# Kernel optimization log

Measured on AMD Instinct MI355X. Metric: run time of the kernel, lower is better.

The kernel has to match this reference:

```python
import jax, jax.numpy as jnp
import numpy as np

N_QUBITS = 4
DIM = 2 ** N_QUBITS  # 16
B = 262144
N_FEATURES = 64


def _apply_ry(state, theta, q):
    # state: (B, 16) complex64; theta: scalar or (B,) angle; RY on wire q (wire 0 = MSB)
    b = state.shape[0]
    L, R = 2 ** q, 2 ** (N_QUBITS - 1 - q)
    s = state.reshape(b, L, 2, R)
    theta = jnp.broadcast_to(jnp.asarray(theta, jnp.float32), (b,))
    c = jnp.cos(theta * 0.5)[:, None, None]
    sn = jnp.sin(theta * 0.5)[:, None, None]
    s0, s1 = s[:, :, 0], s[:, :, 1]
    n0 = c * s0 - sn * s1
    n1 = sn * s0 + c * s1
    return jnp.stack([n0, n1], axis=2).reshape(b, DIM)


def _apply_rz(state, theta, q):
    # RZ(theta) = diag(exp(-i theta/2), exp(+i theta/2)) on wire q
    b = state.shape[0]
    L, R = 2 ** q, 2 ** (N_QUBITS - 1 - q)
    s = state.reshape(b, L, 2, R)
    theta = jnp.broadcast_to(jnp.asarray(theta, jnp.float32), (b,))
    p = jnp.exp(-0.5j * theta)[:, None, None].astype(state.dtype)
    n0 = s[:, :, 0] * p
    n1 = s[:, :, 1] * jnp.conj(p)
    return jnp.stack([n0, n1], axis=2).reshape(b, DIM)


def _cnot(state, c):
    # CNOT with control wire c, target wire c+1 (adjacent, as in the circuit)
    b = state.shape[0]
    L, R = 2 ** c, 2 ** (N_QUBITS - 2 - c)
    s = state.reshape(b, L, 2, 2, R)
    s1 = jnp.flip(s[:, :, 1], axis=2)  # flip target when control=1
    return jnp.stack([s[:, :, 0], s1], axis=2).reshape(b, DIM)


def _simulate(angles, w):
    # angles: (B, 4) input RY rotations; w: (8, 2) trainable gate angles
    b = angles.shape[0]
    state = jnp.zeros((b, DIM), jnp.complex64).at[:, 0].set(1.0)
    for q in range(N_QUBITS):
        state = _apply_ry(state, angles[:, q], q)
    for q in range(N_QUBITS):
        state = _apply_rz(state, w[q, 0], q)
        state = _apply_ry(state, w[q, 1], q)
    for q in range(N_QUBITS - 1):
        state = _cnot(state, q)
    for q in range(N_QUBITS):
        state = _apply_rz(state, w[q + N_QUBITS, 0], q)
        state = _apply_ry(state, w[q + N_QUBITS, 1], q)
    probs = (state.real ** 2 + state.imag ** 2).reshape((b,) + (2,) * N_QUBITS)
    outs = []
    for q in range(N_QUBITS):
        axes = tuple(a for a in range(1, N_QUBITS + 1) if a != q + 1)
        p = probs.sum(axis=axes)  # (B, 2)
        outs.append(p[:, 0] - p[:, 1])  # <Z_q>
    return jnp.stack(outs, axis=1).astype(jnp.float32)


def setup_inputs() -> dict:
    key = jax.random.key(0)
    k1, k2, k3 = jax.random.split(key, 3)
    x = jax.random.normal(k1, (B, N_FEATURES), jnp.float32)
    fm_w = jax.random.normal(k2, (N_QUBITS, N_FEATURES), jnp.float32) / jnp.sqrt(N_FEATURES)
    fm_b = jnp.zeros((N_QUBITS,), jnp.float32)
    # TorchLayer default init: uniform(0, 2*pi)
    q_weights = jax.random.uniform(k3, (2 * N_QUBITS, 2), jnp.float32, 0.0, 2.0 * np.pi)
    return {"x": x, "fm_w": fm_w, "fm_b": fm_b, "q_weights": q_weights}


def reference(x, fm_w, fm_b, q_weights):
    angles = x @ fm_w.T + fm_b  # feature_map Linear(n_features -> n_qubits)
    return _simulate(angles, q_weights)  # (B, n_qubits) Pauli-Z expectations
```

## Files before the change

kernel.cpp:

```cpp
#include <hip/hip_runtime.h>

#define NQ 4
#define DIM 16
#define NPAIR 136

__global__ __launch_bounds__(256) void qnn_prep(const float* __restrict__ w,
                                                float* __restrict__ Apack) {
    __shared__ float Ure[DIM][DIM + 1];
    __shared__ float Uim[DIM][DIM + 1];
    const int tid = threadIdx.x;

    if (tid < DIM) {
        float re[DIM], im[DIM];
#pragma unroll
        for (int k = 0; k < DIM; ++k) { re[k] = (k == tid) ? 1.f : 0.f; im[k] = 0.f; }

#pragma unroll
        for (int layer = 0; layer < 2; ++layer) {
#pragma unroll
            for (int q = 0; q < NQ; ++q) {
                const int bit = 1 << (3 - q);
                const int g = layer * NQ + q;
                float sr, cr;
                sincosf(0.5f * w[g * 2 + 0], &sr, &cr);
#pragma unroll
                for (int k = 0; k < DIM; ++k) {
                    if (!(k & bit)) {
                        const int k1 = k | bit;
                        float r0 = re[k], i0 = im[k], r1 = re[k1], i1 = im[k1];
                        re[k]  = r0 * cr + i0 * sr;  im[k]  = i0 * cr - r0 * sr;
                        re[k1] = r1 * cr - i1 * sr;  im[k1] = i1 * cr + r1 * sr;
                    }
                }
                float sy, cy;
                sincosf(0.5f * w[g * 2 + 1], &sy, &cy);
#pragma unroll
                for (int k = 0; k < DIM; ++k) {
                    if (!(k & bit)) {
                        const int k1 = k | bit;
                        float r0 = re[k], i0 = im[k], r1 = re[k1], i1 = im[k1];
                        re[k]  = cy * r0 - sy * r1;  im[k]  = cy * i0 - sy * i1;
                        re[k1] = sy * r0 + cy * r1;  im[k1] = sy * i0 + cy * i1;
                    }
                }
            }
            if (layer == 0) {
#pragma unroll
                for (int c = 0; c < 3; ++c) {
                    const int cb = 1 << (3 - c), tb = 1 << (2 - c);
#pragma unroll
                    for (int k = 0; k < DIM; ++k) {
                        if ((k & cb) && !(k & tb)) {
                            const int k1 = k | tb;
                            float t;
                            t = re[k]; re[k] = re[k1]; re[k1] = t;
                            t = im[k]; im[k] = im[k1]; im[k1] = t;
                        }
                    }
                }
            }
        }
#pragma unroll
        for (int k = 0; k < DIM; ++k) { Ure[k][tid] = re[k]; Uim[k][tid] = im[k]; }
    }
    __syncthreads();

    if (tid < NPAIR) {
        int i = 0, j = 0, pp = tid;
        for (i = 0; i < DIM; ++i) {
            const int row = DIM - i;
            if (pp < row) { j = i + pp; break; }
            pp -= row;
        }
        const float f = (i == j) ? 1.f : 2.f;
#pragma unroll
        for (int q = 0; q < NQ; ++q) {
            float acc = 0.f;
#pragma unroll
            for (int k = 0; k < DIM; ++k) {
                const float zq = ((k >> (3 - q)) & 1) ? -1.f : 1.f;
                acc += zq * (Ure[k][i] * Ure[k][j] + Uim[k][i] * Uim[k][j]);
            }
            Apack[tid * 4 + q] = f * acc;
        }
    }
}

__global__ __launch_bounds__(256) void qnn_main(const float* __restrict__ x,
                                                const float* __restrict__ fm_w,
                                                const float* __restrict__ fm_b,
                                                const float* __restrict__ Apack,
                                                float* __restrict__ out, int B) {
    const int b = blockIdx.x * 256 + threadIdx.x;
    if (b >= B) return;

    float acc[NQ];
#pragma unroll
    for (int q = 0; q < NQ; ++q) acc[q] = fm_b[q];

    const float4* __restrict__ x4 = (const float4*)(x + (size_t)b * 64);
    const float4* __restrict__ w4 = (const float4*)fm_w;
#pragma unroll
    for (int t = 0; t < 16; ++t) {
        const float4 xv = x4[t];
#pragma unroll
        for (int q = 0; q < NQ; ++q) {
            const float4 wv = w4[q * 16 + t];
            acc[q] += xv.x * wv.x + xv.y * wv.y + xv.z * wv.z + xv.w * wv.w;
        }
    }

    float c[NQ], s[NQ];
#pragma unroll
    for (int q = 0; q < NQ; ++q) __sincosf(0.5f * acc[q], &s[q], &c[q]);

    float p01[4], p23[4];
#pragma unroll
    for (int u = 0; u < 4; ++u) {
        p01[u] = ((u & 2) ? s[0] : c[0]) * ((u & 1) ? s[1] : c[1]);
        p23[u] = ((u & 2) ? s[2] : c[2]) * ((u & 1) ? s[3] : c[3]);
    }
    float st[DIM];
#pragma unroll
    for (int i = 0; i < DIM; ++i) st[i] = p01[i >> 2] * p23[i & 3];

    float o0 = 0.f, o1 = 0.f, o2 = 0.f, o3 = 0.f;
    const float4* __restrict__ A4 = (const float4*)Apack;
    int p = 0;
#pragma unroll
    for (int i = 0; i < DIM; ++i) {
#pragma unroll
        for (int j = i; j < DIM; ++j) {
            const float pr = st[i] * st[j];
            const float4 aq = A4[p];
            o0 += aq.x * pr; o1 += aq.y * pr; o2 += aq.z * pr; o3 += aq.w * pr;
            ++p;
        }
    }

    float4 o = make_float4(o0, o1, o2, o3);
    *(float4*)(out + (size_t)b * 4) = o;
}

extern "C" void kernel_launch(void* const* d_in, const int* in_sizes, int n_in,
                              void* d_out, int out_size, void* d_ws, size_t ws_size,
                              hipStream_t stream) {
    const float* x    = (const float*)d_in[0];
    const float* fm_w = (const float*)d_in[1];
    const float* fm_b = (const float*)d_in[2];
    const float* qw   = (const float*)d_in[3];
    float* out = (float*)d_out;
    float* Apack = (float*)d_ws;

    const int B = in_sizes[0] / 64;

    qnn_prep<<<1, 256, 0, stream>>>(qw, Apack);
    qnn_main<<<(B + 255) / 256, 256, 0, stream>>>(x, fm_w, fm_b, Apack, out, B);
}
```

Measured before the change: 29.16 us.

## Stage x tile through LDS with coalesced float4 loads per block

Each 128-thread block now loads its 128x64 slice of x with coalesced float4 reads across threads, stores it into padded shared memory, then each thread reads its own row from LDS. Before this, each thread loaded a 256-byte contiguous row, so lanes in a wavefront touched addresses far apart. The block size also drops from 256 to 128. The cost is about 34 KB of LDS per block, which may limit occupancy, plus a barrier and extra registers to hold the staged float4s.

```diff
diff --git a/kernel.cpp b/kernel.cpp
--- a/kernel.cpp
+++ b/kernel.cpp
@@ -3,6 +3,8 @@
 #define NQ 4
 #define DIM 16
 #define NPAIR 136
+#define ROWS 128
+#define XPAD 68
 
 __global__ __launch_bounds__(256) void qnn_prep(const float* __restrict__ w,
                                                 float* __restrict__ Apack) {
@@ -86,23 +88,48 @@
     }
 }
 
-__global__ __launch_bounds__(256) void qnn_main(const float* __restrict__ x,
+__global__ __launch_bounds__(128) void qnn_main(const float* __restrict__ x,
                                                 const float* __restrict__ fm_w,
                                                 const float* __restrict__ fm_b,
                                                 const float* __restrict__ Apack,
                                                 float* __restrict__ out, int B) {
-    const int b = blockIdx.x * 256 + threadIdx.x;
+    __shared__ float xs[ROWS * XPAD];
+    const int tid = threadIdx.x;
+    const long long tile = (long long)blockIdx.x * ROWS;
+
+    const float4* __restrict__ xg = (const float4*)(x + tile * 64);
+    const long long rem = (long long)B - tile;
+    float4 r[16];
+    if (rem >= ROWS) {
+#pragma unroll
+        for (int i = 0; i < 16; ++i) r[i] = xg[tid + 128 * i];
+    } else {
+#pragma unroll
+        for (int i = 0; i < 16; ++i) {
+            const int v = tid + 128 * i;
+            r[i] = (v < (int)rem * 16) ? xg[v] : make_float4(0.f, 0.f, 0.f, 0.f);
+        }
+    }
+#pragma unroll
+    for (int i = 0; i < 16; ++i) {
+        const int v = tid + 128 * i;
+        const int rw = v >> 4, c4 = v & 15;
+        *(float4*)&xs[rw * XPAD + c4 * 4] = r[i];
+    }
+    __syncthreads();
+
+    const long long b = tile + tid;
     if (b >= B) return;
 
     float acc[NQ];
 #pragma unroll
     for (int q = 0; q < NQ; ++q) acc[q] = fm_b[q];
 
-    const float4* __restrict__ x4 = (const float4*)(x + (size_t)b * 64);
+    const float4* __restrict__ xr = (const float4*)&xs[tid * XPAD];
     const float4* __restrict__ w4 = (const float4*)fm_w;
 #pragma unroll
     for (int t = 0; t < 16; ++t) {
-        const float4 xv = x4[t];
+        const float4 xv = xr[t];
 #pragma unroll
         for (int q = 0; q < NQ; ++q) {
             const float4 wv = w4[q * 16 + t];
@@ -138,8 +165,7 @@
         }
     }
 
-    float4 o = make_float4(o0, o1, o2, o3);
-    *(float4*)(out + (size_t)b * 4) = o;
+    *(float4*)(out + b * 4) = make_float4(o0, o1, o2, o3);
 }
 
 extern "C" void kernel_launch(void* const* d_in, const int* in_sizes, int n_in,
@@ -155,5 +181,5 @@
     const int B = in_sizes[0] / 64;
 
     qnn_prep<<<1, 256, 0, stream>>>(qw, Apack);
-    qnn_main<<<(B + 255) / 256, 256, 0, stream>>>(x, fm_w, fm_b, Apack, out, B);
+    qnn_main<<<(B + ROWS - 1) / ROWS, 128, 0, stream>>>(x, fm_w, fm_b, Apack, out, B);
 }
```

New measurement: 32.40 us. +11.1%, slower.

## Stage x tiles through LDS via async global_load_lds and parallelize prep kernel

Applied to the files above, without the earlier changes.

The main kernel now copies each block's 128-row tile of x into shared memory with the global_load_lds builtin. The copy is coalesced and rotated so the per-row float4 reads that follow avoid bank conflicts, replacing strided per-thread global float4 loads. The block size drops to 128 threads to match the tile. The prep kernel now spreads the unitary build over 256 threads using wave shuffles and computes the Apack entries across 544 threads instead of 16 and 136 threads doing serial loops. The cost is 32KB of LDS per block, which may lower occupancy, plus a full barrier before any compute starts.

```diff
diff --git a/kernel.cpp b/kernel.cpp
--- a/kernel.cpp
+++ b/kernel.cpp
@@ -3,143 +3,150 @@
 #define NQ 4
 #define DIM 16
 #define NPAIR 136
+#define ROWS 128
 
 __global__ __launch_bounds__(256) void qnn_prep(const float* __restrict__ w,
                                                 float* __restrict__ Apack) {
     __shared__ float Ure[DIM][DIM + 1];
     __shared__ float Uim[DIM][DIM + 1];
     const int tid = threadIdx.x;
+    const int col = tid >> 4, k = tid & 15;
 
-    if (tid < DIM) {
-        float re[DIM], im[DIM];
-#pragma unroll
-        for (int k = 0; k < DIM; ++k) { re[k] = (k == tid) ? 1.f : 0.f; im[k] = 0.f; }
+    float re = (k == col) ? 1.f : 0.f;
+    float im = 0.f;
 
 #pragma unroll
-        for (int layer = 0; layer < 2; ++layer) {
+    for (int layer = 0; layer < 2; ++layer) {
 #pragma unroll
-            for (int q = 0; q < NQ; ++q) {
-                const int bit = 1 << (3 - q);
-                const int g = layer * NQ + q;
-                float sr, cr;
-                sincosf(0.5f * w[g * 2 + 0], &sr, &cr);
-#pragma unroll
-                for (int k = 0; k < DIM; ++k) {
-                    if (!(k & bit)) {
-                        const int k1 = k | bit;
-                        float r0 = re[k], i0 = im[k], r1 = re[k1], i1 = im[k1];
-                        re[k]  = r0 * cr + i0 * sr;  im[k]  = i0 * cr - r0 * sr;
-                        re[k1] = r1 * cr - i1 * sr;  im[k1] = i1 * cr + r1 * sr;
-                    }
-                }
-                float sy, cy;
-                sincosf(0.5f * w[g * 2 + 1], &sy, &cy);
-#pragma unroll
-                for (int k = 0; k < DIM; ++k) {
-                    if (!(k & bit)) {
-                        const int k1 = k | bit;
-                        float r0 = re[k], i0 = im[k], r1 = re[k1], i1 = im[k1];
-                        re[k]  = cy * r0 - sy * r1;  im[k]  = cy * i0 - sy * i1;
-                        re[k1] = sy * r0 + cy * r1;  im[k1] = sy * i0 + cy * i1;
-                    }
-                }
+        for (int q = 0; q < NQ; ++q) {
+            const int bit = 1 << (3 - q);
+            const int g = layer * NQ + q;
+            float sr, cr;
+            sincosf(0.5f * w[g * 2 + 0], &sr, &cr);
+            {
+                const float ssr = (k & bit) ? -sr : sr;
+                const float nre = re * cr + im * ssr;
+                const float nim = im * cr - re * ssr;
+                re = nre; im = nim;
             }
-            if (layer == 0) {
-#pragma unroll
-                for (int c = 0; c < 3; ++c) {
-                    const int cb = 1 << (3 - c), tb = 1 << (2 - c);
-#pragma unroll
-                    for (int k = 0; k < DIM; ++k) {
-                        if ((k & cb) && !(k & tb)) {
-                            const int k1 = k | tb;
-                            float t;
-                            t = re[k]; re[k] = re[k1]; re[k1] = t;
-                            t = im[k]; im[k] = im[k1]; im[k1] = t;
-                        }
-                    }
-                }
+            float sy, cy;
+            sincosf(0.5f * w[g * 2 + 1], &sy, &cy);
+            {
+                const float pre = __shfl_xor(re, bit);
+                const float pim = __shfl_xor(im, bit);
+                const float se = (k & bit) ? sy : -sy;
+                const float nre = cy * re + se * pre;
+                const float nim = cy * im + se * pim;
+                re = nre; im = nim;
             }
         }
+        if (layer == 0) {
 #pragma unroll
-        for (int k = 0; k < DIM; ++k) { Ure[k][tid] = re[k]; Uim[k][tid] = im[k]; }
+            for (int c = 0; c < 3; ++c) {
+                const int cb = 1 << (3 - c), tb = 1 << (2 - c);
+                const float pre = __shfl_xor(re, tb);
+                const float pim = __shfl_xor(im, tb);
+                const bool swap = (k & cb) != 0;
+                re = swap ? pre : re;
+                im = swap ? pim : im;
+            }
+        }
     }
+    Ure[k][col] = re;
+    Uim[k][col] = im;
     __syncthreads();
 
-    if (tid < NPAIR) {
-        int i = 0, j = 0, pp = tid;
+    for (int d = tid; d < NPAIR * 4; d += 256) {
+        const int p = d >> 2, q = d & 3;
+        int i = 0, j = 0, pp = p;
         for (i = 0; i < DIM; ++i) {
             const int row = DIM - i;
             if (pp < row) { j = i + pp; break; }
             pp -= row;
         }
         const float f = (i == j) ? 1.f : 2.f;
+        float acc = 0.f;
 #pragma unroll
-        for (int q = 0; q < NQ; ++q) {
-            float acc = 0.f;
-#pragma unroll
-            for (int k = 0; k < DIM; ++k) {
-                const float zq = ((k >> (3 - q)) & 1) ? -1.f : 1.f;
-                acc += zq * (Ure[k][i] * Ure[k][j] + Uim[k][i] * Uim[k][j]);
-            }
-            Apack[tid * 4 + q] = f * acc;
+        for (int kk = 0; kk < DIM; ++kk) {
+            const float zq = ((kk >> (3 - q)) & 1) ? -1.f : 1.f;
+            acc += zq * (Ure[kk][i] * Ure[kk][j] + Uim[kk][i] * Uim[kk][j]);
         }
+        Apack[d] = f * acc;
     }
 }
 
-__global__ __launch_bounds__(256) void qnn_main(const float* __restrict__ x,
+__global__ __launch_bounds__(128) void qnn_main(const float* __restrict__ x,
                                                 const float* __restrict__ fm_w,
                                                 const float* __restrict__ fm_b,
                                                 const float* __restrict__ Apack,
                                                 float* __restrict__ out, int B) {
-    const int b = blockIdx.x * 256 + threadIdx.x;
-    if (b >= B) return;
+    __shared__ float xs[ROWS * 64];
+    const int tid = threadIdx.x;
+    const long long tile = (long long)blockIdx.x * ROWS;
 
-    float acc[NQ];
+    const float4* __restrict__ xg4 = (const float4*)x + tile * 16;
+    const int wv_id = tid >> 6, l = tid & 63;
 #pragma unroll
-    for (int q = 0; q < NQ; ++q) acc[q] = fm_b[q];
+    for (int i = 0; i < 16; ++i) {
+        const int j = wv_id * 16 + i;
+        const int r = 4 * j + (l >> 4);
+        const int gsrc = ((l & 15) + r) & 15;
+        const float4* src = xg4 + r * 16 + gsrc;
+        float* dst = &xs[j * 256];
+        __builtin_amdgcn_global_load_lds(
+            (const __attribute__((address_space(1))) void*)src,
+            (__attribute__((address_space(3))) void*)dst, 16, 0, 0);
+    }
+    __syncthreads();
 
-    const float4* __restrict__ x4 = (const float4*)(x + (size_t)b * 64);
-    const float4* __restrict__ w4 = (const float4*)fm_w;
+    const long long b = tile + tid;
+    if (b < B) {
+        float acc[NQ];
 #pragma unroll
-    for (int t = 0; t < 16; ++t) {
-        const float4 xv = x4[t];
+        for (int q = 0; q < NQ; ++q) acc[q] = fm_b[q];
+
+        const float4* __restrict__ w4 = (const float4*)fm_w;
 #pragma unroll
-        for (int q = 0; q < NQ; ++q) {
-            const float4 wv = w4[q * 16 + t];
-            acc[q] += xv.x * wv.x + xv.y * wv.y + xv.z * wv.z + xv.w * wv.w;
+        for (int t = 0; t < 16; ++t) {
+            const int s = (t - tid) & 15;
+            const float4 xv = *(const float4*)&xs[tid * 64 + 4 * s];
+#pragma unroll
+            for (int q = 0; q < NQ; ++q) {
+                const float4 wvq = w4[q * 16 + t];
+                acc[q] += xv.x * wvq.x + xv.y * wvq.y + xv.z * wvq.z + xv.w * wvq.w;
+            }
         }
+
+        float c[NQ], s4[NQ];
+#pragma unroll
+        for (int q = 0; q < NQ; ++q) __sincosf(0.5f * acc[q], &s4[q], &c[q]);
+
+        float p01[4], p23[4];
+#pragma unroll
+        for (int u = 0; u < 4; ++u) {
+            p01[u] = ((u & 2) ? s4[0] : c[0]) * ((u & 1) ? s4[1] : c[1]);
+            p23[u] = ((u & 2) ? s4[2] : c[2]) * ((u & 1) ? s4[3] : c[3]);
+        }
+        float st[DIM];
+#pragma unroll
+        for (int i = 0; i < DIM; ++i) st[i] = p01[i >> 2] * p23[i & 3];
+
+        float o0 = 0.f, o1 = 0.f, o2 = 0.f, o3 = 0.f;
+        const float4* __restrict__ A4 = (const float4*)Apack;
+        int p = 0;
+#pragma unroll
+        for (int i = 0; i < DIM; ++i) {
+#pragma unroll
+            for (int j = i; j < DIM; ++j) {
+                const float pr = st[i] * st[j];
+                const float4 aq = A4[p];
+                o0 += aq.x * pr; o1 += aq.y * pr; o2 += aq.z * pr; o3 += aq.w * pr;
+                ++p;
+            }
+        }
+
+        *(float4*)(out + b * 4) = make_float4(o0, o1, o2, o3);
     }
-
-    float c[NQ], s[NQ];
-#pragma unroll
-    for (int q = 0; q < NQ; ++q) __sincosf(0.5f * acc[q], &s[q], &c[q]);
-
-    float p01[4], p23[4];
-#pragma unroll
-    for (int u = 0; u < 4; ++u) {
-        p01[u] = ((u & 2) ? s[0] : c[0]) * ((u & 1) ? s[1] : c[1]);
-        p23[u] = ((u & 2) ? s[2] : c[2]) * ((u & 1) ? s[3] : c[3]);
-    }
-    float st[DIM];
-#pragma unroll
-    for (int i = 0; i < DIM; ++i) st[i] = p01[i >> 2] * p23[i & 3];
-
-    float o0 = 0.f, o1 = 0.f, o2 = 0.f, o3 = 0.f;
-    const float4* __restrict__ A4 = (const float4*)Apack;
-    int p = 0;
-#pragma unroll
-    for (int i = 0; i < DIM; ++i) {
-#pragma unroll
-        for (int j = i; j < DIM; ++j) {
-            const float pr = st[i] * st[j];
-            const float4 aq = A4[p];
-            o0 += aq.x * pr; o1 += aq.y * pr; o2 += aq.z * pr; o3 += aq.w * pr;
-            ++p;
-        }
-    }
-
-    float4 o = make_float4(o0, o1, o2, o3);
-    *(float4*)(out + (size_t)b * 4) = o;
 }
 
 extern "C" void kernel_launch(void* const* d_in, const int* in_sizes, int n_in,
@@ -155,5 +162,5 @@
     const int B = in_sizes[0] / 64;
 
     qnn_prep<<<1, 256, 0, stream>>>(qw, Apack);
-    qnn_main<<<(B + 255) / 256, 256, 0, stream>>>(x, fm_w, fm_b, Apack, out, B);
+    qnn_main<<<(B + ROWS - 1) / ROWS, 128, 0, stream>>>(x, fm_w, fm_b, Apack, out, B);
 }
```

After: 32.65 us. +12.0%, slower.
